# Kernel optimization log

Measured on AMD Instinct MI355X. Metric: run time of the kernel, lower is better.

Reference implementation:

```python
import jax, jax.numpy as jnp
import numpy as np

WH, WW = 12, 12          # window height/width
N = WH * WW              # tokens per window (144)
HEADS = 16
DIM = 1024
C = DIM // 2             # attention channel dim (512)
HEAD_DIM = C // HEADS    # 32


def _rel_pos_index(wh, ww):
    ch, cw = np.arange(wh), np.arange(ww)
    coords = np.stack(np.meshgrid(ch, cw, indexing='ij')).reshape(2, -1)  # [2, N]
    rel = (coords[:, :, None] - coords[:, None, :]).transpose(1, 2, 0)    # [N, N, 2]
    rel = rel.copy()
    rel[:, :, 0] += wh - 1
    rel[:, :, 1] += ww - 1
    rel[:, :, 0] *= 2 * ww - 1
    return rel.sum(-1)  # [N, N] int


def _layernorm(x, g, b, eps=1e-5):
    mu = jnp.mean(x, axis=-1, keepdims=True)
    var = jnp.mean(jnp.square(x - mu), axis=-1, keepdims=True)
    return (x - mu) * jax.lax.rsqrt(var + eps) * g + b


def setup_inputs():
    key = jax.random.key(0)
    ks = jax.random.split(key, 10)
    std = 0.02
    inp = {
        'x': jax.random.normal(ks[0], (256, N, DIM), jnp.float32),
        'template': jax.random.normal(ks[1], (64, N, DIM), jnp.float32),
        'mask0': jnp.zeros((16, N, N), jnp.float32),
        'mask1': jnp.zeros((4, N, N), jnp.float32),
        's_H': 48, 's_W': 48, 't_H': 24, 't_W': 24,
        'rpb_table': jax.random.normal(ks[2], ((2 * WH - 1) * (2 * WW - 1), HEADS), jnp.float32) * std,
        'w_ps': jax.random.normal(ks[3], (DIM, C), jnp.float32) * std,
        'b_ps': jnp.zeros((C,), jnp.float32),
        'g_ps': jnp.ones((C,), jnp.float32),
        'be_ps': jnp.zeros((C,), jnp.float32),
        'w_pt': jax.random.normal(ks[4], (DIM, C), jnp.float32) * std,
        'b_pt': jnp.zeros((C,), jnp.float32),
        'g_pt': jnp.ones((C,), jnp.float32),
        'be_pt': jnp.zeros((C,), jnp.float32),
        'w_qkv': jax.random.normal(ks[5], (C, 3 * C), jnp.float32) * std,
        'b_qkv': jnp.zeros((3 * C,), jnp.float32),
        'w_tr': jax.random.normal(ks[6], (C, DIM), jnp.float32) * std,
        'b_tr': jnp.zeros((DIM,), jnp.float32),
        'w_sr': jax.random.normal(ks[7], (C, DIM), jnp.float32) * std,
        'b_sr': jnp.zeros((DIM,), jnp.float32),
    }
    return inp


def reference(x, template, mask0, mask1, s_H, s_W, t_H, t_W,
              rpb_table, w_ps, b_ps, g_ps, be_ps, w_pt, b_pt, g_pt, be_pt,
              w_qkv, b_qkv, w_tr, b_tr, w_sr, b_sr):
    scale = HEAD_DIM ** (-0.5)
    search_attn = _layernorm(x @ w_ps + b_ps, g_ps, be_ps)          # [Sw, N, C]
    template_attn = _layernorm(template @ w_pt + b_pt, g_pt, be_pt)  # [Tw, N, C]
    Sw, Tw = search_attn.shape[0], template_attn.shape[0]
    xa = jnp.concatenate([template_attn, search_attn], axis=0)      # [B_, N, C]
    B_, n, c = xa.shape

    qkv = (xa @ w_qkv + b_qkv).reshape(B_, n, 3, HEADS, HEAD_DIM)
    q = qkv[:, :, 0].transpose(0, 2, 1, 3) * scale  # [B_, H, N, Dh]
    k = qkv[:, :, 1].transpose(0, 2, 1, 3)
    v = qkv[:, :, 2].transpose(0, 2, 1, 3)

    idx = _rel_pos_index(WH, WW)  # numpy constant [N, N]
    bias = rpb_table[idx.reshape(-1)].reshape(n, n, HEADS).transpose(2, 0, 1)  # [H, N, N]

    attn = jnp.einsum('bhnd,bhmd->bhnm', q, k) + bias[None]  # [B_, H, N, N]

    attn_t, attn_s = attn[:Tw], attn[Tw:]
    nWs = mask0.shape[0]
    attn_s = (attn_s.reshape(Sw // nWs, nWs, HEADS, n, n) + mask0[None, :, None]).reshape(Sw, HEADS, n, n)
    nWt = mask1.shape[0]
    attn_t = (attn_t.reshape(Tw // nWt, nWt, HEADS, n, n) + mask1[None, :, None]).reshape(Tw, HEADS, n, n)
    attn = jax.nn.softmax(jnp.concatenate([attn_t, attn_s], axis=0), axis=-1)

    out = jnp.einsum('bhnm,bhmd->bhnd', attn, v).transpose(0, 2, 1, 3).reshape(B_, n, c)
    template_out = out[:Tw] @ w_tr + b_tr  # [Tw, N, DIM]
    search_out = out[Tw:] @ w_sr + b_sr    # [Sw, N, DIM]
    return (template_out, search_out)
```

## Files before the change

### kernel.cpp

```cpp
#include <hip/hip_runtime.h>


using s16x8 = __attribute__((ext_vector_type(8))) short;
using f32x4 = __attribute__((ext_vector_type(4))) float;
typedef __attribute__((ext_vector_type(2))) unsigned u32x2;

#define NTOK 144
#define NHEADS 16
#define CDIM 512
#define TROWS 9216
#define SROWS 36864
#define TOTROWS 46080
#define NWIN 320
#define NCLS 20

__device__ __forceinline__ unsigned short f2bf(float f) {
  unsigned u = __float_as_uint(f);
  u += 0x7fffu + ((u >> 16) & 1u);
  return (unsigned short)(u >> 16);
}
__device__ __forceinline__ float bf2f(unsigned short u) {
  return __uint_as_float(((unsigned)u) << 16);
}
__device__ __forceinline__ s16x8 mk8(unsigned a, unsigned b, unsigned c, unsigned d) {
  union { unsigned u[4]; s16x8 v; } x;
  x.u[0] = a; x.u[1] = b; x.u[2] = c; x.u[3] = d;
  return x.v;
}

__device__ __forceinline__ void gld16(const void* g, void* l) {
  __builtin_amdgcn_global_load_lds(
      (const __attribute__((address_space(1))) unsigned int*)g,
      (__attribute__((address_space(3))) unsigned int*)l, 16, 0, 0);
}


__global__ void transpose_cast(const float* __restrict__ w,
                               unsigned short* __restrict__ wT, int Kd, int Nd,
                               int nScale, float s) {
  int i = blockIdx.x * 256 + threadIdx.x;
  if (i >= Kd * Nd) return;
  int n = i / Kd, k = i % Kd;
  float v = w[(size_t)k * Nd + n];
  if (n < nScale) v *= s;
  wT[i] = f2bf(v);
}

__global__ void scale_bias(const float* __restrict__ in, float* __restrict__ out) {
  int i = blockIdx.x * 256 + threadIdx.x;
  if (i >= 1536) return;
  out[i] = in[i] * (i < 512 ? 0.17677669529663687f : 1.0f);
}

__global__ __launch_bounds__(256) void cast_bf16(const float* __restrict__ in,
                                                 unsigned short* __restrict__ out, int n8) {
  int i = blockIdx.x * 256 + threadIdx.x;
  if (i >= n8) return;
  const float4* p = (const float4*)in + (size_t)i * 2;
  float4 f0 = p[0], f1 = p[1];
  s16x8 o;
  o[0] = (short)f2bf(f0.x); o[1] = (short)f2bf(f0.y);
  o[2] = (short)f2bf(f0.z); o[3] = (short)f2bf(f0.w);
  o[4] = (short)f2bf(f1.x); o[5] = (short)f2bf(f1.y);
  o[6] = (short)f2bf(f1.z); o[7] = (short)f2bf(f1.w);
  *(s16x8*)&out[(size_t)i * 8] = o;
}

__global__ void build_cmb(const float* __restrict__ rpb, const float* __restrict__ m0,
                          const float* __restrict__ m1, unsigned short* __restrict__ cmb) {
  int i = blockIdx.x * 256 + threadIdx.x;
  if (i >= NCLS * NHEADS * NTOK * NTOK) return;
  int cls = i / (NHEADS * NTOK * NTOK);
  int rem = i % (NHEADS * NTOK * NTOK);
  int h = rem / (NTOK * NTOK);
  int ij = rem % (NTOK * NTOK);
  int qi = ij / NTOK, kj = ij % NTOK;
  int dh = qi / 12 - kj / 12 + 11;
  int dw = qi % 12 - kj % 12 + 11;
  float bias = rpb[(dh * 23 + dw) * NHEADS + h];
  float mv = (cls < 4) ? m1[(size_t)cls * NTOK * NTOK + ij]
                       : m0[(size_t)(cls - 4) * NTOK * NTOK + ij];
  cmb[i] = f2bf(bias + mv);
}

template<int EPI>
__global__ __launch_bounds__(256) void gemm_glds(
    const unsigned short* __restrict__ Ab,
    const unsigned short* __restrict__ BTt, const unsigned short* __restrict__ BTs,
    const float* __restrict__ biast, const float* __restrict__ biass,
    void* __restrict__ Cout, int M, int N, int K)
{
  __shared__ short As[2][128 * 64];
  __shared__ short Bs[2][128 * 64];
  const int t = threadIdx.x;
  const int lane = t & 63, wv = t >> 6, lg = lane >> 4, lc = lane & 15;

  const int id = blockIdx.x + gridDim.x * blockIdx.y;
  const int chunk = (gridDim.x * gridDim.y) >> 3;
  const int lid = (id & 7) * chunk + (id >> 3);
  const int bn = (lid % gridDim.x) * 128, bm = (lid / gridDim.x) * 128;

  const bool isT = bm < TROWS;
  const unsigned short* BT = isT ? BTt : BTs;
  const float* bias = isT ? biast : biass;

  const int srow = 32 * wv + (lane >> 3);
  const int scol = ((lane & 7) ^ ((lane >> 3) & 7)) * 8;
  const unsigned short* aSrc = Ab + (size_t)(bm + srow) * K + scol;
  const unsigned short* bSrc = BT + (size_t)(bn + srow) * K + scol;
  const size_t rowK8 = (size_t)8 * K;

  f32x4 acc[2][8] = {};

  auto STAGE = [&](int b, int kt) {
#pragma unroll
    for (int i = 0; i < 4; i++) {
      gld16(aSrc + kt + i * rowK8, &As[b][(wv * 4 + i) * 512]);
      gld16(bSrc + kt + i * rowK8, &Bs[b][(wv * 4 + i) * 512]);
    }
  };
  auto COMPUTE = [&](int b) {
#pragma unroll
    for (int kk = 0; kk < 2; kk++) {
      const int csw = 8 * ((4 * kk + lg) ^ (lc & 7));
      const int r0 = wv * 32 + lc, r1 = r0 + 16;
      s16x8 a0 = *(const s16x8*)&As[b][r0 * 64 + csw];
      s16x8 a1 = *(const s16x8*)&As[b][r1 * 64 + csw];
#pragma unroll
      for (int nt = 0; nt < 8; nt++) {
        s16x8 bfr = *(const s16x8*)&Bs[b][(nt * 16 + lc) * 64 + csw];
        acc[0][nt] = __builtin_amdgcn_mfma_f32_16x16x32_bf16(a0, bfr, acc[0][nt], 0, 0, 0);
        acc[1][nt] = __builtin_amdgcn_mfma_f32_16x16x32_bf16(a1, bfr, acc[1][nt], 0, 0, 0);
      }
    }
  };

  STAGE(0, 0);
  int cur = 0;
  for (int kt = 64; kt < K; kt += 64) {
    STAGE(cur ^ 1, kt);
    asm volatile("s_waitcnt vmcnt(8)" ::: "memory");
    __builtin_amdgcn_s_barrier();
    __builtin_amdgcn_sched_barrier(0);
    COMPUTE(cur);
    __builtin_amdgcn_s_barrier();
    cur ^= 1;
  }
  asm volatile("s_waitcnt vmcnt(0)" ::: "memory");
  __builtin_amdgcn_s_barrier();
  __builtin_amdgcn_sched_barrier(0);
  COMPUTE(cur);

#pragma unroll
  for (int mt = 0; mt < 2; mt++) {
    const int rbase = bm + wv * 32 + mt * 16 + lg * 4;
#pragma unroll
    for (int nt = 0; nt < 8; nt++) {
      const int cg = bn + nt * 16 + lc;
#pragma unroll
      for (int r = 0; r < 4; r++) {
        const int rg = rbase + r;
        float val = acc[mt][nt][r] + bias[cg];
        if (EPI == 2) ((float*)Cout)[(size_t)rg * N + cg] = val;
        else ((unsigned short*)Cout)[(size_t)rg * N + cg] = f2bf(val);
      }
    }
  }
}

__global__ __launch_bounds__(256) void ln_kernel(
    unsigned short* __restrict__ xa,
    const float* __restrict__ g_pt, const float* __restrict__ be_pt,
    const float* __restrict__ g_ps, const float* __restrict__ be_ps)
{
  const int row = blockIdx.x * 4 + (threadIdx.x >> 6);
  const int lane = threadIdx.x & 63;
  const bool isT = row < TROWS;
  const float* gg = isT ? g_pt : g_ps;
  const float* be = isT ? be_pt : be_ps;
  unsigned short* p = xa + (size_t)row * CDIM;
  const int c0 = lane * 8;

  s16x8 v8 = *(const s16x8*)&p[c0];
  float f[8];
  float s = 0.f, s2 = 0.f;
#pragma unroll
  for (int i = 0; i < 8; i++) {
    float xv = bf2f((unsigned short)v8[i]);
    f[i] = xv; s += xv; s2 += xv * xv;
  }
#pragma unroll
  for (int d = 1; d < 64; d <<= 1) { s += __shfl_xor(s, d); s2 += __shfl_xor(s2, d); }
  float mu = s * (1.f / CDIM);
  float var = s2 * (1.f / CDIM) - mu * mu;
  float rs = rsqrtf(var + 1e-5f);

  float4 g0 = *(const float4*)&gg[c0], g1 = *(const float4*)&gg[c0 + 4];
  float4 e0 = *(const float4*)&be[c0], e1 = *(const float4*)&be[c0 + 4];
  float gv[8] = {g0.x, g0.y, g0.z, g0.w, g1.x, g1.y, g1.z, g1.w};
  float ev[8] = {e0.x, e0.y, e0.z, e0.w, e1.x, e1.y, e1.z, e1.w};
  s16x8 o;
#pragma unroll
  for (int i = 0; i < 8; i++)
    o[i] = (short)f2bf((f[i] - mu) * rs * gv[i] + ev[i]);
  *(s16x8*)&p[c0] = o;
}

__global__ __launch_bounds__(576) void attn_kernel(
    const unsigned short* __restrict__ qkv, const unsigned short* __restrict__ cmb,
    unsigned short* __restrict__ outp)
{
  __shared__ short VT[32 * 168];
  const int nb = NWIN * NHEADS;
  const int lid = (blockIdx.x & 7) * (nb >> 3) + (blockIdx.x >> 3);
  const int w = lid >> 4, h = lid & 15;
  const int t = threadIdx.x;
  const unsigned short* qb = qkv + (size_t)w * NTOK * 1536;
  const int hq = h * 32;

  {
    const int n = t >> 2, d0 = (t & 3) * 8;
    s16x8 vv = *(const s16x8*)&qb[(size_t)n * 1536 + 1024 + hq + d0];
#pragma unroll
    for (int i = 0; i < 8; i++) VT[(d0 + i) * 168 + n] = vv[i];
  }
  if (t < 512) VT[(t >> 4) * 168 + 144 + (t & 15)] = 0;

  const int lane = t & 63, wv = t >> 6, lg = lane >> 4, lc = lane & 15;
  const int q = wv * 16 + lc;
  const f32x4 zero = {0.f, 0.f, 0.f, 0.f};

  const s16x8 qf = *(const s16x8*)&qb[(size_t)q * 1536 + hq + lg * 8];

  const int cls = (w < 64) ? (w & 3) : 4 + ((w - 64) & 15);
  const unsigned short* cm =
      cmb + ((size_t)cls * NHEADS + h) * (NTOK * NTOK) + (size_t)q * NTOK;
  uint2 cmr[9];
#pragma unroll
  for (int nt = 0; nt < 9; nt++)
    cmr[nt] = *(const uint2*)&cm[nt * 16 + lg * 4];

  f32x4 accS[9];
  __builtin_amdgcn_s_setprio(1);
#pragma unroll
  for (int nt = 0; nt < 9; nt++) {
    s16x8 kf = *(const s16x8*)&qb[(size_t)(nt * 16 + lc) * 1536 + 512 + hq + lg * 8];
    accS[nt] = __builtin_amdgcn_mfma_f32_16x16x32_bf16(kf, qf, zero, 0, 0, 0);
  }
  __builtin_amdgcn_s_setprio(0);

  float mx = -1e30f;
#pragma unroll
  for (int nt = 0; nt < 9; nt++) {
    accS[nt][0] += bf2f((unsigned short)(cmr[nt].x & 0xffff));
    accS[nt][1] += bf2f((unsigned short)(cmr[nt].x >> 16));
    accS[nt][2] += bf2f((unsigned short)(cmr[nt].y & 0xffff));
    accS[nt][3] += bf2f((unsigned short)(cmr[nt].y >> 16));
#pragma unroll
    for (int r = 0; r < 4; r++) mx = fmaxf(mx, accS[nt][r]);
  }
  mx = fmaxf(mx, __shfl_xor(mx, 16));
  mx = fmaxf(mx, __shfl_xor(mx, 32));

  float sum = 0.f;
#pragma unroll
  for (int nt = 0; nt < 9; nt++)
#pragma unroll
    for (int r = 0; r < 4; r++) {
      float e = __expf(accS[nt][r] - mx);
      accS[nt][r] = e;
      sum += e;
    }
  sum += __shfl_xor(sum, 16);
  sum += __shfl_xor(sum, 32);
  const float inv = 1.f / sum;

  unsigned pk0[9], pk1[9];
#pragma unroll
  for (int nt = 0; nt < 9; nt++) {
    pk0[nt] = (unsigned)f2bf(accS[nt][0]) | ((unsigned)f2bf(accS[nt][1]) << 16);
    pk1[nt] = (unsigned)f2bf(accS[nt][2]) | ((unsigned)f2bf(accS[nt][3]) << 16);
  }

  __syncthreads();

  __builtin_amdgcn_s_setprio(1);
#pragma unroll
  for (int dt = 0; dt < 2; dt++) {
    const short* vbase = &VT[(dt * 16 + lc) * 168];
    f32x4 accO = zero;
#pragma unroll
    for (int kk = 0; kk < 4; kk++) {
      u32x2 A0 = *(const u32x2*)&vbase[32 * kk + lg * 4];
      u32x2 A1 = *(const u32x2*)&vbase[32 * kk + 16 + lg * 4];
      s16x8 a = mk8(A0[0], A0[1], A1[0], A1[1]);
      s16x8 b = mk8(pk0[2 * kk], pk1[2 * kk], pk0[2 * kk + 1], pk1[2 * kk + 1]);
      accO = __builtin_amdgcn_mfma_f32_16x16x32_bf16(a, b, accO, 0, 0, 0);
    }
    {
      u32x2 A0 = *(const u32x2*)&vbase[128 + lg * 4];
      s16x8 a = mk8(A0[0], A0[1], 0u, 0u);
      s16x8 b = mk8(pk0[8], pk1[8], 0u, 0u);
      accO = __builtin_amdgcn_mfma_f32_16x16x32_bf16(a, b, accO, 0, 0, 0);
    }
    unsigned o0 = (unsigned)f2bf(accO[0] * inv) | ((unsigned)f2bf(accO[1] * inv) << 16);
    unsigned o1 = (unsigned)f2bf(accO[2] * inv) | ((unsigned)f2bf(accO[3] * inv) << 16);
    uint2 st; st.x = o0; st.y = o1;
    *(uint2*)&outp[(size_t)(w * NTOK + q) * CDIM + hq + dt * 16 + lg * 4] = st;
  }
  __builtin_amdgcn_s_setprio(0);
}

extern "C" void kernel_launch(void* const* d_in, const int* in_sizes, int n_in,
                              void* d_out, int out_size, void* d_ws, size_t ws_size,
                              hipStream_t stream)
{
  const float* x     = (const float*)d_in[0];
  const float* tpl   = (const float*)d_in[1];
  const float* mask0 = (const float*)d_in[2];
  const float* mask1 = (const float*)d_in[3];
  const float* rpb   = (const float*)d_in[8];
  const float* w_ps  = (const float*)d_in[9];
  const float* b_ps  = (const float*)d_in[10];
  const float* g_ps  = (const float*)d_in[11];
  const float* be_ps = (const float*)d_in[12];
  const float* w_pt  = (const float*)d_in[13];
  const float* b_pt  = (const float*)d_in[14];
  const float* g_pt  = (const float*)d_in[15];
  const float* be_pt = (const float*)d_in[16];
  const float* w_qkv = (const float*)d_in[17];
  const float* b_qkv = (const float*)d_in[18];
  const float* w_tr  = (const float*)d_in[19];
  const float* b_tr  = (const float*)d_in[20];
  const float* w_sr  = (const float*)d_in[21];
  const float* b_sr  = (const float*)d_in[22];

  char* ws = (char*)d_ws;
  unsigned short* wpsT  = (unsigned short*)(ws + 0x0000000);
  unsigned short* wptT  = (unsigned short*)(ws + 0x0100000);
  unsigned short* wqkvT = (unsigned short*)(ws + 0x0200000);
  unsigned short* wtrT  = (unsigned short*)(ws + 0x0380000);
  unsigned short* wsrT  = (unsigned short*)(ws + 0x0480000);
  unsigned short* cmb   = (unsigned short*)(ws + 0x0580000);
  float* bqS            = (float*)(ws + 0x12F0000);
  unsigned short* xa    = (unsigned short*)(ws + 0x1300000);
  unsigned short* Sa    = (unsigned short*)(ws + 0x4000000);
  unsigned short* qkvF  = (unsigned short*)(ws + 0x4000000);
  float* outb           = (float*)d_out;

  transpose_cast<<<2048, 256, 0, stream>>>(w_ps, wpsT, 1024, 512, 0, 1.f);
  transpose_cast<<<2048, 256, 0, stream>>>(w_pt, wptT, 1024, 512, 0, 1.f);
  transpose_cast<<<3072, 256, 0, stream>>>(w_qkv, wqkvT, 512, 1536,
                                           512, 0.17677669529663687f);
  transpose_cast<<<2048, 256, 0, stream>>>(w_tr, wtrT, 512, 1024, 0, 1.f);
  transpose_cast<<<2048, 256, 0, stream>>>(w_sr, wsrT, 512, 1024, 0, 1.f);
  scale_bias<<<6, 256, 0, stream>>>(b_qkv, bqS);
  build_cmb<<<(NCLS * NHEADS * NTOK * NTOK + 255) / 256, 256, 0, stream>>>(rpb, mask0, mask1, cmb);

  cast_bf16<<<(TROWS * 1024 / 8 + 255) / 256, 256, 0, stream>>>(tpl, Sa, TROWS * 1024 / 8);
  cast_bf16<<<(SROWS * 1024 / 8 + 255) / 256, 256, 0, stream>>>(
      x, Sa + (size_t)TROWS * 1024, SROWS * 1024 / 8);

  gemm_glds<0><<<dim3(4, 360), 256, 0, stream>>>(Sa, wptT, wpsT, b_pt, b_ps,
                                                 xa, TOTROWS, CDIM, 1024);
  ln_kernel<<<TOTROWS / 4, 256, 0, stream>>>(xa, g_pt, be_pt, g_ps, be_ps);

  gemm_glds<0><<<dim3(12, 360), 256, 0, stream>>>(xa, wqkvT, wqkvT, bqS, bqS,
                                                  qkvF, TOTROWS, 1536, CDIM);
  attn_kernel<<<NWIN * NHEADS, 576, 0, stream>>>(qkvF, cmb, xa);

  gemm_glds<2><<<dim3(8, 360), 256, 0, stream>>>(xa, wtrT, wsrT, b_tr, b_sr,
                                                 outb, TOTROWS, 1024, CDIM);
}
```

Baseline: 466.1 us.

## Enlarge GEMM tiles to 256x256 with 8-wave blocks and dynamic LDS

Replaces the 128x128, 4-wave bf16 MFMA GEMM with a 256x256 tile computed by 8 waves in a 2x4 layout. Each wave now holds an 8x4 grid of 16x16 accumulators, and the double-buffered A and B tiles move into 128KB of dynamic shared memory. The aim is more data reuse per LDS and global load and fewer blocks for all three projection GEMMs. In exchange, register pressure is higher, only one block fits per CU, and the first GEMM launches just 360 blocks, which risks wave-quantization tail effects.

```diff
diff --git a/kernel.cpp b/kernel.cpp
--- a/kernel.cpp
+++ b/kernel.cpp
@@ -84,21 +84,21 @@
 }
 
 template<int EPI>
-__global__ __launch_bounds__(256) void gemm_glds(
+__global__ __launch_bounds__(512, 2) void gemm256(
     const unsigned short* __restrict__ Ab,
     const unsigned short* __restrict__ BTt, const unsigned short* __restrict__ BTs,
     const float* __restrict__ biast, const float* __restrict__ biass,
     void* __restrict__ Cout, int M, int N, int K)
 {
-  __shared__ short As[2][128 * 64];
-  __shared__ short Bs[2][128 * 64];
+  extern __shared__ short smem[];
   const int t = threadIdx.x;
   const int lane = t & 63, wv = t >> 6, lg = lane >> 4, lc = lane & 15;
+  const int wr = wv >> 2, wc = wv & 3;
 
   const int id = blockIdx.x + gridDim.x * blockIdx.y;
   const int chunk = (gridDim.x * gridDim.y) >> 3;
   const int lid = (id & 7) * chunk + (id >> 3);
-  const int bn = (lid % gridDim.x) * 128, bm = (lid / gridDim.x) * 128;
+  const int bn = (lid % gridDim.x) * 256, bm = (lid / gridDim.x) * 256;
 
   const bool isT = bm < TROWS;
   const unsigned short* BT = isT ? BTt : BTs;
@@ -110,27 +110,33 @@
   const unsigned short* bSrc = BT + (size_t)(bn + srow) * K + scol;
   const size_t rowK8 = (size_t)8 * K;
 
-  f32x4 acc[2][8] = {};
+  f32x4 acc[8][4] = {};
 
   auto STAGE = [&](int b, int kt) {
+    short* Asb = smem + b * 16384;
+    short* Bsb = smem + 32768 + b * 16384;
 #pragma unroll
     for (int i = 0; i < 4; i++) {
-      gld16(aSrc + kt + i * rowK8, &As[b][(wv * 4 + i) * 512]);
-      gld16(bSrc + kt + i * rowK8, &Bs[b][(wv * 4 + i) * 512]);
+      gld16(aSrc + kt + i * rowK8, Asb + (wv * 4 + i) * 512);
+      gld16(bSrc + kt + i * rowK8, Bsb + (wv * 4 + i) * 512);
     }
   };
   auto COMPUTE = [&](int b) {
+    const short* Asb = smem + b * 16384;
+    const short* Bsb = smem + 32768 + b * 16384;
 #pragma unroll
     for (int kk = 0; kk < 2; kk++) {
       const int csw = 8 * ((4 * kk + lg) ^ (lc & 7));
-      const int r0 = wv * 32 + lc, r1 = r0 + 16;
-      s16x8 a0 = *(const s16x8*)&As[b][r0 * 64 + csw];
-      s16x8 a1 = *(const s16x8*)&As[b][r1 * 64 + csw];
-#pragma unroll
-      for (int nt = 0; nt < 8; nt++) {
-        s16x8 bfr = *(const s16x8*)&Bs[b][(nt * 16 + lc) * 64 + csw];
-        acc[0][nt] = __builtin_amdgcn_mfma_f32_16x16x32_bf16(a0, bfr, acc[0][nt], 0, 0, 0);
-        acc[1][nt] = __builtin_amdgcn_mfma_f32_16x16x32_bf16(a1, bfr, acc[1][nt], 0, 0, 0);
+      s16x8 bf[4];
+#pragma unroll
+      for (int c = 0; c < 4; c++)
+        bf[c] = *(const s16x8*)&Bsb[(wc * 64 + c * 16 + lc) * 64 + csw];
+#pragma unroll
+      for (int r = 0; r < 8; r++) {
+        s16x8 af = *(const s16x8*)&Asb[(wr * 128 + r * 16 + lc) * 64 + csw];
+#pragma unroll
+        for (int c = 0; c < 4; c++)
+          acc[r][c] = __builtin_amdgcn_mfma_f32_16x16x32_bf16(af, bf[c], acc[r][c], 0, 0, 0);
       }
     }
   };
@@ -152,17 +158,16 @@
   COMPUTE(cur);
 
 #pragma unroll
-  for (int mt = 0; mt < 2; mt++) {
-    const int rbase = bm + wv * 32 + mt * 16 + lg * 4;
-#pragma unroll
-    for (int nt = 0; nt < 8; nt++) {
-      const int cg = bn + nt * 16 + lc;
-#pragma unroll
-      for (int r = 0; r < 4; r++) {
-        const int rg = rbase + r;
-        float val = acc[mt][nt][r] + bias[cg];
-        if (EPI == 2) ((float*)Cout)[(size_t)rg * N + cg] = val;
-        else ((unsigned short*)Cout)[(size_t)rg * N + cg] = f2bf(val);
+  for (int r = 0; r < 8; r++) {
+    const int rbase = bm + wr * 128 + r * 16 + lg * 4;
+#pragma unroll
+    for (int c = 0; c < 4; c++) {
+      const int cg = bn + wc * 64 + c * 16 + lc;
+#pragma unroll
+      for (int rr = 0; rr < 4; rr++) {
+        float val = acc[r][c][rr] + bias[cg];
+        if (EPI == 2) ((float*)Cout)[(size_t)(rbase + rr) * N + cg] = val;
+        else ((unsigned short*)Cout)[(size_t)(rbase + rr) * N + cg] = f2bf(val);
       }
     }
   }
@@ -348,6 +353,11 @@
   unsigned short* qkvF  = (unsigned short*)(ws + 0x4000000);
   float* outb           = (float*)d_out;
 
+  hipFuncSetAttribute((const void*)gemm256<0>,
+                      hipFuncAttributeMaxDynamicSharedMemorySize, 131072);
+  hipFuncSetAttribute((const void*)gemm256<2>,
+                      hipFuncAttributeMaxDynamicSharedMemorySize, 131072);
+
   transpose_cast<<<2048, 256, 0, stream>>>(w_ps, wpsT, 1024, 512, 0, 1.f);
   transpose_cast<<<2048, 256, 0, stream>>>(w_pt, wptT, 1024, 512, 0, 1.f);
   transpose_cast<<<3072, 256, 0, stream>>>(w_qkv, wqkvT, 512, 1536,
@@ -361,14 +371,14 @@
   cast_bf16<<<(SROWS * 1024 / 8 + 255) / 256, 256, 0, stream>>>(
       x, Sa + (size_t)TROWS * 1024, SROWS * 1024 / 8);
 
-  gemm_glds<0><<<dim3(4, 360), 256, 0, stream>>>(Sa, wptT, wpsT, b_pt, b_ps,
-                                                 xa, TOTROWS, CDIM, 1024);
+  gemm256<0><<<dim3(2, 180), 512, 131072, stream>>>(Sa, wptT, wpsT, b_pt, b_ps,
+                                                    xa, TOTROWS, CDIM, 1024);
   ln_kernel<<<TOTROWS / 4, 256, 0, stream>>>(xa, g_pt, be_pt, g_ps, be_ps);
 
-  gemm_glds<0><<<dim3(12, 360), 256, 0, stream>>>(xa, wqkvT, wqkvT, bqS, bqS,
-                                                  qkvF, TOTROWS, 1536, CDIM);
+  gemm256<0><<<dim3(6, 180), 512, 131072, stream>>>(xa, wqkvT, wqkvT, bqS, bqS,
+                                                    qkvF, TOTROWS, 1536, CDIM);
   attn_kernel<<<NWIN * NHEADS, 576, 0, stream>>>(qkvF, cmb, xa);
 
-  gemm_glds<2><<<dim3(8, 360), 256, 0, stream>>>(xa, wtrT, wsrT, b_tr, b_sr,
-                                                 outb, TOTROWS, 1024, CDIM);
-}
+  gemm256<2><<<dim3(4, 180), 512, 131072, stream>>>(xa, wtrT, wsrT, b_tr, b_sr,
+                                                    outb, TOTROWS, 1024, CDIM);
+}
```

New measurement: 453.1 us. 1.03x faster.
